# Optimization experiments

Measured on AMD Instinct MI355X. Metric: run time of the kernel, lower is better.

## Reference

```python
import jax, jax.numpy as jnp
import numpy as np

B, NV, NP, D, K = 8, 2048, 4096, 64, 8  # shapes per batch, vtx/pts counts, feat dim, num_interp
NEG = -1e9


def _unit(x):
    return x / jnp.clip(jnp.linalg.norm(x, axis=-1, keepdims=True), 1e-12)


def _gather(v, idx):
    # v: [B, N, C], idx: [B, Q, K] -> [B, Q, K, C]
    return jax.vmap(lambda a, i: a[i])(v, idx)


def setup_inputs() -> dict:
    key = jax.random.key(0)
    k1, k2, k3, k4, k5 = jax.random.split(key, 5)
    return {
        "vtx": jax.random.normal(k1, (B * NV, 3), jnp.float32),
        "pts": jax.random.normal(k2, (B * NP, 3), jnp.float32),
        "vtx_feature": jax.random.normal(k3, (B * NV, D), jnp.float32),
        "pts_feature": jax.random.normal(k4, (B * NP, D), jnp.float32),
        "vismask_logits": jax.random.normal(k5, (B * NV, 1), jnp.float32),
    }


def reference(vtx, pts, vtx_feature, pts_feature, vismask_logits):
    # --- per-batch min-max normalization of sigmoid(vismask) (serial loop in torch) ---
    vm = jax.nn.sigmoid(vismask_logits).reshape(B, NV, 1)
    vmin = vm.min(axis=1, keepdims=True)
    vmax = vm.max(axis=1, keepdims=True)
    vm = (vm - vmin) / (vmax - vmin)

    vtxb = vtx.reshape(B, NV, 3)
    ptsb = pts.reshape(B, NP, 3)
    vf = vtx_feature.reshape(B, NV, D)
    pf = pts_feature.reshape(B, NP, D)

    # --- cosine KNN: for each vtx, k nearest pts by cosine similarity ---
    sim = jnp.einsum('bnd,bmd->bnm', _unit(vf), _unit(pf))  # [B,NV,NP]
    _, idx = jax.lax.top_k(sim, K)                           # [B,NV,K]

    nbr_pts = _gather(ptsb, idx)                             # [B,NV,K,3]
    nbr_pf = _gather(pf, idx)                                # [B,NV,K,D]
    euclid = nbr_pts - vtxb[:, :, None, :]
    # raw (unnormalized) dot product, weighted by vismask of the query vertex
    fsim = jnp.sum(nbr_pf * vf[:, :, None, :], axis=-1, keepdims=True) * vm[:, :, None, :]
    # scatter_add over assign_index[0] == sum over the K grouped neighbors
    flow_init = jnp.sum(euclid * fsim, axis=2) / jnp.sum(fsim, axis=2)  # [B,NV,3]

    # --- interpolate flow at invisible vertices from visible ones (2nd cosine KNN) ---
    vis = vm >= 0.5                                          # [B,NV,1]
    vfn = _unit(vf)
    sim2 = jnp.einsum('bnd,bmd->bnm', vfn, vfn)              # [B,NV,NV]
    sim2 = jnp.where(vis[:, :, 0][:, None, :], sim2, NEG)    # keys restricted to visible vtx
    _, idx2 = jax.lax.top_k(sim2, K)                         # [B,NV,K]

    nbr_vf = _gather(vf, idx2)                               # [B,NV,K,D]
    nbr_flow = _gather(flow_init, idx2)                      # [B,NV,K,3]
    fsim2 = jnp.sum(nbr_vf * vf[:, :, None, :], axis=-1, keepdims=True)
    invis_flow = jnp.sum(nbr_flow * fsim2, axis=2) / jnp.sum(fsim2, axis=2)

    flow = jnp.where(vis, flow_init, invis_flow)             # flow_init[invis] = invis_flow
    l1_points = jnp.concatenate([flow, vm], axis=-1)         # [B,NV,4]
    return l1_points.reshape(B * NV, 4)
```

## Files before the change

### kernel.cpp

```cpp
#include <hip/hip_runtime.h>
#include <math.h>

#define BB 8
#define NVV 2048
#define NPP 4096
#define DD 64
#define NQ (BB * NVV)
#define QT (NQ / 16)
#define NC1 2
#define NC2 2

typedef __attribute__((ext_vector_type(8))) short short8;
typedef __attribute__((ext_vector_type(8))) unsigned short ushort8;
typedef __attribute__((ext_vector_type(4))) float f32x4;


__device__ __forceinline__ unsigned short bf16rn(float x) {
  unsigned u = __float_as_uint(x);
  return (unsigned short)((u + 0x7FFFu + ((u >> 16) & 1u)) >> 16);
}
__device__ __forceinline__ float bf2f(unsigned short h) {
  return __uint_as_float(((unsigned)h) << 16);
}

__device__ __forceinline__ void net8(unsigned* a, unsigned v) {
#pragma unroll
  for (int k = 0; k < 7; k++) {
    unsigned r;
    asm("v_med3_u32 %0, %1, %2, %3" : "=v"(r) : "v"(v), "v"(a[k]), "v"(a[k + 1]));
    a[k] = r;
  }
  a[7] = a[7] > v ? a[7] : v;
}

__device__ __forceinline__ void ins8(float* tv, int* ti, float v, int id) {
  bool c1 = v > tv[1], c2 = v > tv[2], c3 = v > tv[3];
  bool c4 = v > tv[4], c5 = v > tv[5], c6 = v > tv[6], c7 = v > tv[7];
  tv[0] = c1 ? tv[1] : v;                ti[0] = c1 ? ti[1] : id;
  tv[1] = c2 ? tv[2] : (c1 ? v : tv[1]); ti[1] = c2 ? ti[2] : (c1 ? id : ti[1]);
  tv[2] = c3 ? tv[3] : (c2 ? v : tv[2]); ti[2] = c3 ? ti[3] : (c2 ? id : ti[2]);
  tv[3] = c4 ? tv[4] : (c3 ? v : tv[3]); ti[3] = c4 ? ti[4] : (c3 ? id : ti[3]);
  tv[4] = c5 ? tv[5] : (c4 ? v : tv[4]); ti[4] = c5 ? ti[5] : (c4 ? id : ti[4]);
  tv[5] = c6 ? tv[6] : (c5 ? v : tv[5]); ti[5] = c6 ? ti[6] : (c5 ? id : ti[5]);
  tv[6] = c7 ? tv[7] : (c6 ? v : tv[6]); ti[6] = c7 ? ti[7] : (c6 ? id : ti[6]);
  tv[7] = c7 ? v : tv[7];                ti[7] = c7 ? id : ti[7];
}

__global__ __launch_bounds__(256) void k_prep(const float* __restrict__ logits,
                                              const float* __restrict__ vf,
                                              const float* __restrict__ pf,
                                              float* __restrict__ vm,
                                              float* __restrict__ inv_vf,
                                              float* __restrict__ inv_pf,
                                              unsigned short* __restrict__ qhi,
                                              unsigned short* __restrict__ qlo,
                                              unsigned short* __restrict__ khi,
                                              unsigned short* __restrict__ klo,
                                              float* __restrict__ out) {
  int bid = blockIdx.x, t = threadIdx.x;
  if (bid < BB) {
    int b = bid;
    __shared__ float smn[4], smx[4];
    float vals[8];
    float mn = 1e30f, mx = -1e30f;
#pragma unroll
    for (int i = 0; i < 8; i++) {
      float x = logits[b * NVV + t + i * 256];
      float s = 1.0f / (1.0f + expf(-x));
      vals[i] = s;
      mn = fminf(mn, s);
      mx = fmaxf(mx, s);
    }
    for (int o = 32; o; o >>= 1) {
      mn = fminf(mn, __shfl_xor(mn, o, 64));
      mx = fmaxf(mx, __shfl_xor(mx, o, 64));
    }
    int w = t >> 6;
    if ((t & 63) == 0) { smn[w] = mn; smx[w] = mx; }
    __syncthreads();
    mn = fminf(fminf(smn[0], smn[1]), fminf(smn[2], smn[3]));
    mx = fmaxf(fmaxf(smx[0], smx[1]), fmaxf(smx[2], smx[3]));
    float range = mx - mn;
#pragma unroll
    for (int i = 0; i < 8; i++) {
      float v = (vals[i] - mn) / range;
      int g = b * NVV + t + i * 256;
      vm[g] = v;
      out[g * 4 + 3] = v;
    }
  } else if (bid < BB + 3072) {
    int T = (bid - BB) * 256 + t;
    int row = T >> 4, c = T & 15;
    const float* src;
    float* dst;
    int r;
    if (row < NQ) { src = vf; dst = inv_vf; r = row; }
    else { src = pf; dst = inv_pf; r = row - NQ; }
    float4 v = *(const float4*)(src + (size_t)r * DD + c * 4);
    float s = v.x * v.x + v.y * v.y + v.z * v.z + v.w * v.w;
#pragma unroll
    for (int m = 1; m <= 8; m <<= 1) s += __shfl_xor(s, m, 64);
    if (c == 0) dst[r] = 1.0f / fmaxf(sqrtf(s), 1e-12f);
  } else {
    int T = (bid - BB - 3072) * 256 + t;
    const float* src;
    unsigned short *dh, *dl;
    int s;
    if (T < QT * 128) { s = T; src = vf; dh = qhi; dl = qlo; }
    else { s = T - QT * 128; src = pf; dh = khi; dl = klo; }
    int lane = s & 63, kk = (s >> 6) & 1, tile = s >> 7;
    size_t off = (size_t)(tile * 16 + (lane & 15)) * DD + kk * 32 + ((lane >> 4) & 3) * 8;
    float4 a = *(const float4*)(src + off);
    float4 b = *(const float4*)(src + off + 4);
    float xs[8] = {a.x, a.y, a.z, a.w, b.x, b.y, b.z, b.w};
    ushort8 h, l;
#pragma unroll
    for (int j = 0; j < 8; j++) {
      unsigned short hj = bf16rn(xs[j]);
      h[j] = hj;
      l[j] = bf16rn(xs[j] - bf2f(hj));
    }
    *(ushort8*)(dh + (size_t)s * 8) = h;
    *(ushort8*)(dl + (size_t)s * 8) = l;
  }
}

__global__ __launch_bounds__(256)
void k_knn(const unsigned short* __restrict__ qhi, const unsigned short* __restrict__ qlo,
           const unsigned short* __restrict__ khi, const unsigned short* __restrict__ klo,
           const float* __restrict__ inv_vf, const float* __restrict__ inv_pf,
           const float* __restrict__ vm,
           unsigned* __restrict__ pc1, unsigned* __restrict__ pc2) {
  int wid = (blockIdx.x * 256 + threadIdx.x) >> 6;
  int lane = threadIdx.x & 63, col = lane & 15, quad = lane >> 4;

  const unsigned short *BH, *BL;
  const float *inv, *mask;
  unsigned* PC;
  int qt_g, bt0, row0, ckb, ntiles;
  if (wid < QT * NC1) {
    int ck = wid & (NC1 - 1);
    qt_g = wid / NC1;
    int batch = qt_g >> 7;
    BH = khi; BL = klo;
    inv = inv_pf + batch * NPP;
    mask = nullptr;
    ntiles = 256 / NC1;
    bt0 = batch * 256 + ck * ntiles;
    PC = pc1;
    row0 = ck * 8; ckb = ck * ntiles;
  } else {
    int w = wid - QT * NC1;
    int ck = w & (NC2 - 1);
    qt_g = w / NC2;
    int batch = qt_g >> 7;
    BH = qhi; BL = qlo;
    inv = inv_vf + batch * NVV;
    mask = vm + batch * NVV;
    ntiles = 128 / NC2;
    bt0 = batch * 128 + ck * ntiles;
    PC = pc2;
    row0 = ck * 8; ckb = ck * ntiles;
  }

  size_t ab = (size_t)qt_g * 1024 + lane * 8;
  short8 ah0 = *(const short8*)(qhi + ab);
  short8 ah1 = *(const short8*)(qhi + ab + 512);
  short8 al0 = *(const short8*)(qlo + ab);
  short8 al1 = *(const short8*)(qlo + ab + 512);

  unsigned tv[4][8];
#pragma unroll
  for (int r = 0; r < 4; r++)
#pragma unroll
    for (int k = 0; k < 8; k++) tv[r][k] = 0u;

#pragma unroll 2
  for (int kt = 0; kt < ntiles; kt++) {
    size_t bo = (size_t)(bt0 + kt) * 1024 + lane * 8;
    short8 bh0 = *(const short8*)(BH + bo);
    short8 bh1 = *(const short8*)(BH + bo + 512);
    short8 bl0 = *(const short8*)(BL + bo);
    short8 bl1 = *(const short8*)(BL + bo + 512);
    int key = (ckb + kt) * 16 + col;
    float iv = inv[key];
    bool ok = mask ? (mask[key] >= 0.5f) : true;
    f32x4 c0 = {0.f, 0.f, 0.f, 0.f}, c1 = {0.f, 0.f, 0.f, 0.f};
    c0 = __builtin_amdgcn_mfma_f32_16x16x32_bf16(ah0, bh0, c0, 0, 0, 0);
    c1 = __builtin_amdgcn_mfma_f32_16x16x32_bf16(ah1, bh1, c1, 0, 0, 0);
    c0 = __builtin_amdgcn_mfma_f32_16x16x32_bf16(ah0, bl0, c0, 0, 0, 0);
    c1 = __builtin_amdgcn_mfma_f32_16x16x32_bf16(ah1, bl1, c1, 0, 0, 0);
    c0 = __builtin_amdgcn_mfma_f32_16x16x32_bf16(al0, bh0, c0, 0, 0, 0);
    c1 = __builtin_amdgcn_mfma_f32_16x16x32_bf16(al1, bh1, c1, 0, 0, 0);
#pragma unroll
    for (int r = 0; r < 4; r++) {
      float s = (c0[r] + c1[r]) * iv;
      unsigned u = (unsigned)fmaxf(fmaf(s, 16384.0f, 262144.0f), 0.0f);
      unsigned pk = (u << 12) | (unsigned)key;
      pk = ok ? pk : 0u;
      net8(tv[r], pk);
    }
  }

#pragma unroll
  for (int m = 1; m <= 8; m <<= 1) {
#pragma unroll
    for (int r = 0; r < 4; r++) {
      unsigned ov[8];
#pragma unroll
      for (int k = 0; k < 8; k++) ov[k] = (unsigned)__shfl_xor((int)tv[r][k], m, 64);
#pragma unroll
      for (int k = 7; k >= 0; k--) net8(tv[r], ov[k]);
    }
  }

  if (col == 0) {
#pragma unroll
    for (int r = 0; r < 4; r++) {
      int q = qt_g * 16 + quad * 4 + r;
#pragma unroll
      for (int k = 0; k < 8; k++)
        PC[(size_t)(row0 + k) * NQ + q] = tv[r][k];
    }
  }
}

__device__ __forceinline__ float dot64(const float4* __restrict__ a,
                                       const float4* __restrict__ b) {
  float a0 = 0.f, a1 = 0.f, a2 = 0.f, a3 = 0.f;
#pragma unroll
  for (int c = 0; c < 16; c++) {
    float4 x = a[c], y = b[c];
    a0 = fmaf(x.x, y.x, a0);
    a1 = fmaf(x.y, y.y, a1);
    a2 = fmaf(x.z, y.z, a2);
    a3 = fmaf(x.w, y.w, a3);
  }
  return (a0 + a1) + (a2 + a3);
}

__global__ __launch_bounds__(256) void k_merge_flow(const unsigned* __restrict__ pc,
                                                    const float* __restrict__ vf,
                                                    const float* __restrict__ pf,
                                                    const float* __restrict__ pts,
                                                    const float* __restrict__ vtx,
                                                    const float* __restrict__ inv_pf,
                                                    float* __restrict__ flow_ws,
                                                    float* __restrict__ out) {
  int T = blockIdx.x * 256 + threadIdx.x;
  int q = T >> 4, c = T & 15, batch = q >> 11;
  const float4* qp = (const float4*)(vf + (size_t)q * DD);
  float tv[8];
  int ti[8];
#pragma unroll
  for (int k = 0; k < 8; k++) { tv[k] = -3.0e38f; ti[k] = 0; }
  {
    unsigned pk = pc[(size_t)c * NQ + q];
    int id = (int)(pk & 0xFFFu);
    int prow = batch * NPP + id;
    float s = dot64(qp, (const float4*)(pf + (size_t)prow * DD)) * inv_pf[prow];
    ins8(tv, ti, s, id);
  }
#pragma unroll
  for (int m = 1; m <= 8; m <<= 1) {
    float ov[8];
    int oi[8];
#pragma unroll
    for (int k = 0; k < 8; k++) {
      ov[k] = __shfl_xor(tv[k], m, 64);
      oi[k] = __shfl_xor(ti[k], m, 64);
    }
#pragma unroll
    for (int k = 7; k >= 0; k--)
      if (ov[k] > tv[0]) ins8(tv, ti, ov[k], oi[k]);
  }
  int id = ti[0];
#pragma unroll
  for (int k = 1; k < 8; k++) id = (c == k) ? ti[k] : id;

  float ax = 0.f, ay = 0.f, az = 0.f, den = 0.f;
  if (c < 8) {
    int prow = batch * NPP + id;
    float w = dot64(qp, (const float4*)(pf + (size_t)prow * DD));
    ax = (pts[prow * 3 + 0] - vtx[q * 3 + 0]) * w;
    ay = (pts[prow * 3 + 1] - vtx[q * 3 + 1]) * w;
    az = (pts[prow * 3 + 2] - vtx[q * 3 + 2]) * w;
    den = w;
  }
#pragma unroll
  for (int m = 1; m <= 8; m <<= 1) {
    ax += __shfl_xor(ax, m, 64);
    ay += __shfl_xor(ay, m, 64);
    az += __shfl_xor(az, m, 64);
    den += __shfl_xor(den, m, 64);
  }
  if (c == 0) {
    float fx = ax / den, fy = ay / den, fz = az / den;
    flow_ws[q * 4 + 0] = fx;
    flow_ws[q * 4 + 1] = fy;
    flow_ws[q * 4 + 2] = fz;
    out[q * 4 + 0] = fx;
    out[q * 4 + 1] = fy;
    out[q * 4 + 2] = fz;
  }
}

__global__ __launch_bounds__(256) void k_merge_final(const unsigned* __restrict__ pc,
                                                     const float* __restrict__ vf,
                                                     const float* __restrict__ vm,
                                                     const float* __restrict__ inv_vf,
                                                     const float* __restrict__ flow_ws,
                                                     float* __restrict__ out) {
  int T = blockIdx.x * 256 + threadIdx.x;
  int q = T >> 4, c = T & 15, batch = q >> 11;
  if (vm[q] >= 0.5f) return;
  const float4* qp = (const float4*)(vf + (size_t)q * DD);
  float tv[8];
  int ti[8];
#pragma unroll
  for (int k = 0; k < 8; k++) { tv[k] = -3.0e38f; ti[k] = 0; }
  {
    unsigned pk = pc[(size_t)c * NQ + q];
    if (pk > 0xFFFu) {
      int id = (int)(pk & 0xFFFu);
      int krow = batch * NVV + id;
      float s = dot64(qp, (const float4*)(vf + (size_t)krow * DD)) * inv_vf[krow];
      ins8(tv, ti, s, id);
    }
  }
#pragma unroll
  for (int m = 1; m <= 8; m <<= 1) {
    float ov[8];
    int oi[8];
#pragma unroll
    for (int k = 0; k < 8; k++) {
      ov[k] = __shfl_xor(tv[k], m, 64);
      oi[k] = __shfl_xor(ti[k], m, 64);
    }
#pragma unroll
    for (int k = 7; k >= 0; k--)
      if (ov[k] > tv[0]) ins8(tv, ti, ov[k], oi[k]);
  }
  int id = ti[0];
#pragma unroll
  for (int k = 1; k < 8; k++) id = (c == k) ? ti[k] : id;

  float ax = 0.f, ay = 0.f, az = 0.f, den = 0.f;
  if (c < 8) {
    int krow = batch * NVV + id;
    float w = dot64(qp, (const float4*)(vf + (size_t)krow * DD));
    ax = flow_ws[krow * 4 + 0] * w;
    ay = flow_ws[krow * 4 + 1] * w;
    az = flow_ws[krow * 4 + 2] * w;
    den = w;
  }
#pragma unroll
  for (int m = 1; m <= 8; m <<= 1) {
    ax += __shfl_xor(ax, m, 64);
    ay += __shfl_xor(ay, m, 64);
    az += __shfl_xor(az, m, 64);
    den += __shfl_xor(den, m, 64);
  }
  if (c == 0) {
    out[q * 4 + 0] = ax / den;
    out[q * 4 + 1] = ay / den;
    out[q * 4 + 2] = az / den;
  }
}

extern "C" void kernel_launch(void* const* d_in, const int* in_sizes, int n_in,
                              void* d_out, int out_size, void* d_ws, size_t ws_size,
                              hipStream_t stream) {
  const float* vtx = (const float*)d_in[0];
  const float* pts = (const float*)d_in[1];
  const float* vf = (const float*)d_in[2];
  const float* pf = (const float*)d_in[3];
  const float* lg = (const float*)d_in[4];
  float* out = (float*)d_out;
  float* ws = (float*)d_ws;

  float* vm = ws;
  float* inv_vf = ws + 16384;
  float* inv_pf = ws + 32768;
  float* flow = ws + 65536;
  unsigned* pc1 = (unsigned*)(ws + 131072);
  unsigned* pc2 = (unsigned*)(ws + 393216);
  unsigned short* qhi = (unsigned short*)(ws + 655360);
  unsigned short* qlo = (unsigned short*)(ws + 1179648);
  unsigned short* khi = (unsigned short*)(ws + 1703936);
  unsigned short* klo = (unsigned short*)(ws + 2752512);

  k_prep<<<BB + 3072 + 1536, 256, 0, stream>>>(lg, vf, pf, vm, inv_vf, inv_pf,
                                               qhi, qlo, khi, klo, out);
  k_knn<<<(QT * NC1 + QT * NC2) / 4, 256, 0, stream>>>(qhi, qlo, khi, klo,
                                                       inv_vf, inv_pf, vm, pc1, pc2);
  k_merge_flow<<<NQ * 16 / 256, 256, 0, stream>>>(pc1, vf, pf, pts, vtx,
                                                  inv_pf, flow, out);
  k_merge_final<<<NQ * 16 / 256, 256, 0, stream>>>(pc2, vf, vm, inv_vf, flow, out);
}
```

Before: 193.0 us.

## Split first KNN over four key chunks and reuse rescored similarity in merge

The point-KNN search now splits the key dimension into four chunks per query tile instead of two, so more waves run the MFMA top-k in parallel, and the merge kernel uses 32 lanes per query to combine 32 candidate lists. The 16384 quantization scale is folded into the stored inverse norms, which removes one multiply per score. The merge kernels recover the neighbour weight from the already computed cosine score times the norm, instead of a second 64-wide dot product. In exchange the merge does more shuffle rounds and the workspace layout grows, and the recovered weights can differ slightly in rounding from the direct dot products.

```diff
diff --git a/kernel.cpp b/kernel.cpp
--- a/kernel.cpp
+++ b/kernel.cpp
@@ -7,7 +7,7 @@
 #define DD 64
 #define NQ (BB * NVV)
 #define QT (NQ / 16)
-#define NC1 2
+#define NC1 4
 #define NC2 2
 
 typedef __attribute__((ext_vector_type(8))) short short8;
@@ -50,8 +50,8 @@
                                               const float* __restrict__ vf,
                                               const float* __restrict__ pf,
                                               float* __restrict__ vm,
-                                              float* __restrict__ inv_vf,
-                                              float* __restrict__ inv_pf,
+                                              float* __restrict__ inv_vf_s,
+                                              float* __restrict__ inv_pf_s,
                                               unsigned short* __restrict__ qhi,
                                               unsigned short* __restrict__ qlo,
                                               unsigned short* __restrict__ khi,
@@ -94,13 +94,13 @@
     const float* src;
     float* dst;
     int r;
-    if (row < NQ) { src = vf; dst = inv_vf; r = row; }
-    else { src = pf; dst = inv_pf; r = row - NQ; }
+    if (row < NQ) { src = vf; dst = inv_vf_s; r = row; }
+    else { src = pf; dst = inv_pf_s; r = row - NQ; }
     float4 v = *(const float4*)(src + (size_t)r * DD + c * 4);
     float s = v.x * v.x + v.y * v.y + v.z * v.z + v.w * v.w;
 #pragma unroll
     for (int m = 1; m <= 8; m <<= 1) s += __shfl_xor(s, m, 64);
-    if (c == 0) dst[r] = 1.0f / fmaxf(sqrtf(s), 1e-12f);
+    if (c == 0) dst[r] = 16384.0f / fmaxf(sqrtf(s), 1e-12f);
   } else {
     int T = (bid - BB - 3072) * 256 + t;
     const float* src;
@@ -128,7 +128,7 @@
 __global__ __launch_bounds__(256)
 void k_knn(const unsigned short* __restrict__ qhi, const unsigned short* __restrict__ qlo,
            const unsigned short* __restrict__ khi, const unsigned short* __restrict__ klo,
-           const float* __restrict__ inv_vf, const float* __restrict__ inv_pf,
+           const float* __restrict__ inv_vf_s, const float* __restrict__ inv_pf_s,
            const float* __restrict__ vm,
            unsigned* __restrict__ pc1, unsigned* __restrict__ pc2) {
   int wid = (blockIdx.x * 256 + threadIdx.x) >> 6;
@@ -137,30 +137,28 @@
   const unsigned short *BH, *BL;
   const float *inv, *mask;
   unsigned* PC;
-  int qt_g, bt0, row0, ckb, ntiles;
+  int qt_g, bt0, row0, ckb;
   if (wid < QT * NC1) {
     int ck = wid & (NC1 - 1);
-    qt_g = wid / NC1;
+    qt_g = wid >> 2;
     int batch = qt_g >> 7;
     BH = khi; BL = klo;
-    inv = inv_pf + batch * NPP;
+    inv = inv_pf_s + batch * NPP;
     mask = nullptr;
-    ntiles = 256 / NC1;
-    bt0 = batch * 256 + ck * ntiles;
+    bt0 = batch * 256 + ck * 64;
     PC = pc1;
-    row0 = ck * 8; ckb = ck * ntiles;
+    row0 = ck * 8; ckb = ck * 64;
   } else {
     int w = wid - QT * NC1;
     int ck = w & (NC2 - 1);
-    qt_g = w / NC2;
+    qt_g = w >> 1;
     int batch = qt_g >> 7;
     BH = qhi; BL = qlo;
-    inv = inv_vf + batch * NVV;
+    inv = inv_vf_s + batch * NVV;
     mask = vm + batch * NVV;
-    ntiles = 128 / NC2;
-    bt0 = batch * 128 + ck * ntiles;
+    bt0 = batch * 128 + ck * 64;
     PC = pc2;
-    row0 = ck * 8; ckb = ck * ntiles;
+    row0 = ck * 8; ckb = ck * 64;
   }
 
   size_t ab = (size_t)qt_g * 1024 + lane * 8;
@@ -176,7 +174,7 @@
     for (int k = 0; k < 8; k++) tv[r][k] = 0u;
 
 #pragma unroll 2
-  for (int kt = 0; kt < ntiles; kt++) {
+  for (int kt = 0; kt < 64; kt++) {
     size_t bo = (size_t)(bt0 + kt) * 1024 + lane * 8;
     short8 bh0 = *(const short8*)(BH + bo);
     short8 bh1 = *(const short8*)(BH + bo + 512);
@@ -194,8 +192,8 @@
     c1 = __builtin_amdgcn_mfma_f32_16x16x32_bf16(al1, bh1, c1, 0, 0, 0);
 #pragma unroll
     for (int r = 0; r < 4; r++) {
-      float s = (c0[r] + c1[r]) * iv;
-      unsigned u = (unsigned)fmaxf(fmaf(s, 16384.0f, 262144.0f), 0.0f);
+      float s2 = c0[r] + c1[r];
+      unsigned u = (unsigned)fmaxf(fmaf(s2, iv, 262144.0f), 0.0f);
       unsigned pk = (u << 12) | (unsigned)key;
       pk = ok ? pk : 0u;
       net8(tv[r], pk);
@@ -244,11 +242,11 @@
                                                     const float* __restrict__ pf,
                                                     const float* __restrict__ pts,
                                                     const float* __restrict__ vtx,
-                                                    const float* __restrict__ inv_pf,
+                                                    const float* __restrict__ inv_pf_s,
                                                     float* __restrict__ flow_ws,
                                                     float* __restrict__ out) {
   int T = blockIdx.x * 256 + threadIdx.x;
-  int q = T >> 4, c = T & 15, batch = q >> 11;
+  int q = T >> 5, c = T & 31, batch = q >> 11;
   const float4* qp = (const float4*)(vf + (size_t)q * DD);
   float tv[8];
   int ti[8];
@@ -258,11 +256,12 @@
     unsigned pk = pc[(size_t)c * NQ + q];
     int id = (int)(pk & 0xFFFu);
     int prow = batch * NPP + id;
-    float s = dot64(qp, (const float4*)(pf + (size_t)prow * DD)) * inv_pf[prow];
+    float s = dot64(qp, (const float4*)(pf + (size_t)prow * DD)) *
+              inv_pf_s[prow] * 6.103515625e-5f;
     ins8(tv, ti, s, id);
   }
 #pragma unroll
-  for (int m = 1; m <= 8; m <<= 1) {
+  for (int m = 1; m <= 16; m <<= 1) {
     float ov[8];
     int oi[8];
 #pragma unroll
@@ -275,20 +274,24 @@
       if (ov[k] > tv[0]) ins8(tv, ti, ov[k], oi[k]);
   }
   int id = ti[0];
-#pragma unroll
-  for (int k = 1; k < 8; k++) id = (c == k) ? ti[k] : id;
+  float sv = tv[0];
+#pragma unroll
+  for (int k = 1; k < 8; k++) {
+    id = (c == k) ? ti[k] : id;
+    sv = (c == k) ? tv[k] : sv;
+  }
 
   float ax = 0.f, ay = 0.f, az = 0.f, den = 0.f;
   if (c < 8) {
     int prow = batch * NPP + id;
-    float w = dot64(qp, (const float4*)(pf + (size_t)prow * DD));
+    float w = sv * 16384.0f / inv_pf_s[prow];
     ax = (pts[prow * 3 + 0] - vtx[q * 3 + 0]) * w;
     ay = (pts[prow * 3 + 1] - vtx[q * 3 + 1]) * w;
     az = (pts[prow * 3 + 2] - vtx[q * 3 + 2]) * w;
     den = w;
   }
 #pragma unroll
-  for (int m = 1; m <= 8; m <<= 1) {
+  for (int m = 1; m <= 16; m <<= 1) {
     ax += __shfl_xor(ax, m, 64);
     ay += __shfl_xor(ay, m, 64);
     az += __shfl_xor(az, m, 64);
@@ -308,7 +311,7 @@
 __global__ __launch_bounds__(256) void k_merge_final(const unsigned* __restrict__ pc,
                                                      const float* __restrict__ vf,
                                                      const float* __restrict__ vm,
-                                                     const float* __restrict__ inv_vf,
+                                                     const float* __restrict__ inv_vf_s,
                                                      const float* __restrict__ flow_ws,
                                                      float* __restrict__ out) {
   int T = blockIdx.x * 256 + threadIdx.x;
@@ -324,7 +327,8 @@
     if (pk > 0xFFFu) {
       int id = (int)(pk & 0xFFFu);
       int krow = batch * NVV + id;
-      float s = dot64(qp, (const float4*)(vf + (size_t)krow * DD)) * inv_vf[krow];
+      float s = dot64(qp, (const float4*)(vf + (size_t)krow * DD)) *
+                inv_vf_s[krow] * 6.103515625e-5f;
       ins8(tv, ti, s, id);
     }
   }
@@ -342,13 +346,17 @@
       if (ov[k] > tv[0]) ins8(tv, ti, ov[k], oi[k]);
   }
   int id = ti[0];
-#pragma unroll
-  for (int k = 1; k < 8; k++) id = (c == k) ? ti[k] : id;
+  float sv = tv[0];
+#pragma unroll
+  for (int k = 1; k < 8; k++) {
+    id = (c == k) ? ti[k] : id;
+    sv = (c == k) ? tv[k] : sv;
+  }
 
   float ax = 0.f, ay = 0.f, az = 0.f, den = 0.f;
   if (c < 8) {
     int krow = batch * NVV + id;
-    float w = dot64(qp, (const float4*)(vf + (size_t)krow * DD));
+    float w = sv * 16384.0f / inv_vf_s[krow];
     ax = flow_ws[krow * 4 + 0] * w;
     ay = flow_ws[krow * 4 + 1] * w;
     az = flow_ws[krow * 4 + 2] * w;
@@ -380,21 +388,21 @@
   float* ws = (float*)d_ws;
 
   float* vm = ws;
-  float* inv_vf = ws + 16384;
-  float* inv_pf = ws + 32768;
+  float* inv_vf_s = ws + 16384;
+  float* inv_pf_s = ws + 32768;
   float* flow = ws + 65536;
   unsigned* pc1 = (unsigned*)(ws + 131072);
-  unsigned* pc2 = (unsigned*)(ws + 393216);
-  unsigned short* qhi = (unsigned short*)(ws + 655360);
-  unsigned short* qlo = (unsigned short*)(ws + 1179648);
-  unsigned short* khi = (unsigned short*)(ws + 1703936);
-  unsigned short* klo = (unsigned short*)(ws + 2752512);
-
-  k_prep<<<BB + 3072 + 1536, 256, 0, stream>>>(lg, vf, pf, vm, inv_vf, inv_pf,
+  unsigned* pc2 = (unsigned*)(ws + 655360);
+  unsigned short* qhi = (unsigned short*)(ws + 917504);
+  unsigned short* qlo = (unsigned short*)(ws + 1441792);
+  unsigned short* khi = (unsigned short*)(ws + 1966080);
+  unsigned short* klo = (unsigned short*)(ws + 3014656);
+
+  k_prep<<<BB + 3072 + 1536, 256, 0, stream>>>(lg, vf, pf, vm, inv_vf_s, inv_pf_s,
                                                qhi, qlo, khi, klo, out);
   k_knn<<<(QT * NC1 + QT * NC2) / 4, 256, 0, stream>>>(qhi, qlo, khi, klo,
-                                                       inv_vf, inv_pf, vm, pc1, pc2);
-  k_merge_flow<<<NQ * 16 / 256, 256, 0, stream>>>(pc1, vf, pf, pts, vtx,
-                                                  inv_pf, flow, out);
-  k_merge_final<<<NQ * 16 / 256, 256, 0, stream>>>(pc2, vf, vm, inv_vf, flow, out);
-}
+                                                       inv_vf_s, inv_pf_s, vm, pc1, pc2);
+  k_merge_flow<<<NQ * 32 / 256, 256, 0, stream>>>(pc1, vf, pf, pts, vtx,
+                                                  inv_pf_s, flow, out);
+  k_merge_final<<<NQ * 16 / 256, 256, 0, stream>>>(pc2, vf, vm, inv_vf_s, flow, out);
+}
```

After: 206.1 us. +6.8%, slower.
